# Performance work log

Measured on AMD Instinct MI355X. Metric: run time of the kernel, lower is better.

The kernel has to match this reference:

```python
import jax, jax.numpy as jnp
import numpy as np

N = 50000
E = 800000
IN_C = 128
OUT_C = 128
N_TYPES = 3
NEG_SLOPE = 0.2  # PyG GATConv default negative_slope


def setup_inputs() -> dict:
    key = jax.random.key(0)
    ks = jax.random.split(key, 10)
    x = jax.random.normal(ks[0], (N, IN_C), dtype=jnp.float32)
    edge_index = jax.random.randint(ks[1], (2, E), 0, N, dtype=jnp.int32)
    edge_type = jax.random.randint(ks[2], (E,), 0, N_TYPES, dtype=jnp.int32)
    node_type = jax.random.randint(ks[3], (N,), 0, 3, dtype=jnp.int32)
    s = 1.0 / np.sqrt(IN_C)
    emb_table = jax.random.normal(ks[4], (3, IN_C), dtype=jnp.float32)
    W = jax.random.normal(ks[5], (N_TYPES, IN_C, OUT_C), dtype=jnp.float32) * s
    att_src = jax.random.normal(ks[6], (N_TYPES, OUT_C), dtype=jnp.float32) * s
    att_dst = jax.random.normal(ks[7], (N_TYPES, OUT_C), dtype=jnp.float32) * s
    bias = jax.random.normal(ks[8], (N_TYPES, OUT_C), dtype=jnp.float32) * 0.01
    return {"x": x, "edge_index": edge_index, "edge_type": edge_type,
            "node_type": node_type, "emb_table": emb_table, "W": W,
            "att_src": att_src, "att_dst": att_dst, "bias": bias}


def reference(x, edge_index, edge_type, node_type, emb_table, W, att_src, att_dst, bias):
    # Eval mode: dropouts are identity. edge_index is non-empty -> GAT branch.
    n = x.shape[0]
    x = x + emb_table[node_type]  # node-type embedding add
    src, dst = edge_index[0], edge_index[1]
    out_sum = jnp.zeros((n, OUT_C), dtype=x.dtype)
    for t in range(N_TYPES):  # per-edge-type GATConv (heads=1, add_self_loops=True)
        xw = x @ W[t]                       # [N, out]
        a_s = xw @ att_src[t]               # [N] alpha_src per node
        a_d = xw @ att_dst[t]               # [N] alpha_dst per node
        mask = edge_type == t               # [E]
        e_raw = jax.nn.leaky_relu(a_s[src] + a_d[dst], NEG_SLOPE)  # [E]
        e_self = jax.nn.leaky_relu(a_s + a_d, NEG_SLOPE)           # [N] self-loop logit
        e_masked = jnp.where(mask, e_raw, -jnp.inf)
        m = jnp.maximum(jax.ops.segment_max(e_masked, dst, num_segments=n), e_self)
        m = jax.lax.stop_gradient(m)
        w_edge = jnp.where(mask, jnp.exp(e_raw - m[dst]), 0.0)     # [E]
        w_self = jnp.exp(e_self - m)                               # [N]
        denom = jax.ops.segment_sum(w_edge, dst, num_segments=n) + w_self
        num = jax.ops.segment_sum(w_edge[:, None] * xw[src], dst, num_segments=n) \
              + w_self[:, None] * xw
        out_sum = out_sum + num / denom[:, None] + bias[t]
        # (attention weights per type are w_edge/denom[dst]; only node output returned)
    return out_sum
```

## Files before the change

### kernel.cpp

```cpp
#include <hip/hip_runtime.h>
#include <math.h>

#define N_NODES 50000
#define N_EDGES 800000
#define C 128
#define NT 3
#define NEG 0.2f
#define CAP 64

typedef __attribute__((ext_vector_type(8))) short short8;
typedef __attribute__((ext_vector_type(4))) float f32x4;

__device__ __forceinline__ float leaky(float v) { return v > 0.f ? v : NEG * v; }

__device__ __forceinline__ unsigned short f2bf(float f) {
  unsigned int u = __float_as_uint(f);
  u = (u + 0x7FFFu + ((u >> 16) & 1u)) >> 16;
  return (unsigned short)u;
}
__device__ __forceinline__ float bf_lo(unsigned int w) { return __uint_as_float(w << 16); }
__device__ __forceinline__ float bf_hi(unsigned int w) { return __uint_as_float(w & 0xFFFF0000u); }

__global__ void k_x2(const float* __restrict__ x, const int* __restrict__ node_type,
                     const float* __restrict__ emb, unsigned short* __restrict__ x2b) {
  int i4 = blockIdx.x * 256 + threadIdx.x;
  if (i4 >= N_NODES * (C / 4)) return;
  int node = i4 >> 5;
  int q = i4 & 31;
  int nt = node_type[node];
  float4 xv = ((const float4*)x)[i4];
  float4 ev = ((const float4*)emb)[nt * 32 + q];
  ushort4 o;
  o.x = f2bf(xv.x + ev.x); o.y = f2bf(xv.y + ev.y);
  o.z = f2bf(xv.z + ev.z); o.w = f2bf(xv.w + ev.w);
  ((ushort4*)x2b)[i4] = o;
}

__global__ void k_wt(const float* __restrict__ W, unsigned short* __restrict__ Wt) {
  int n = blockIdx.x, t = blockIdx.y, k = threadIdx.x;
  Wt[((size_t)t * C + n) * C + k] = f2bf(W[((size_t)t * C + k) * C + n]);
}

__global__ void k_gemm(const unsigned short* __restrict__ x2b, const unsigned short* __restrict__ Wt,
                       unsigned short* __restrict__ xwb,
                       const float* __restrict__ att_src, const float* __restrict__ att_dst,
                       float* __restrict__ a_s, float2* __restrict__ ad_es) {
  __shared__ unsigned short As[64][136];
  __shared__ unsigned short Bs[128][136];
  const int tid = threadIdx.x;
  const int wid = tid >> 6, lane = tid & 63;
  const int m = lane & 15, quad = lane >> 4;
  const int row0 = blockIdx.x * 64;
  const int t = blockIdx.z;

#pragma unroll
  for (int it = 0; it < 4; ++it) {
    int c = tid + it * 256;
    int r = c >> 4, kc = c & 15;
    uint4 v = make_uint4(0, 0, 0, 0);
    if (row0 + r < N_NODES) v = *(const uint4*)(x2b + ((size_t)(row0 + r)) * C + kc * 8);
    *(uint4*)&As[r][kc * 8] = v;
  }
  const unsigned short* Wtt = Wt + (size_t)t * C * C;
#pragma unroll
  for (int it = 0; it < 8; ++it) {
    int c = tid + it * 256;
    int n = c >> 4, kc = c & 15;
    *(uint4*)&Bs[n][kc * 8] = *(const uint4*)(Wtt + (size_t)n * C + kc * 8);
  }
  __syncthreads();

  f32x4 acc[8] = {};
#pragma unroll
  for (int k0 = 0; k0 < 128; k0 += 32) {
    short8 a = *(const short8*)&As[wid * 16 + m][k0 + quad * 8];
#pragma unroll
    for (int j = 0; j < 8; ++j) {
      short8 b = *(const short8*)&Bs[j * 16 + m][k0 + quad * 8];
      acc[j] = __builtin_amdgcn_mfma_f32_16x16x32_bf16(a, b, acc[j], 0, 0, 0);
    }
  }

  float asv[8], adv[8];
#pragma unroll
  for (int j = 0; j < 8; ++j) {
    asv[j] = att_src[t * C + j * 16 + m];
    adv[j] = att_dst[t * C + j * 16 + m];
  }
  float ps[4] = {}, pd[4] = {};
#pragma unroll
  for (int j = 0; j < 8; ++j) {
#pragma unroll
    for (int reg = 0; reg < 4; ++reg) {
      int row = row0 + wid * 16 + quad * 4 + reg;
      float v = acc[j][reg];
      if (row < N_NODES) xwb[((size_t)t * N_NODES + row) * C + j * 16 + m] = f2bf(v);
      ps[reg] += v * asv[j];
      pd[reg] += v * adv[j];
    }
  }
#pragma unroll
  for (int off = 1; off < 16; off <<= 1) {
#pragma unroll
    for (int reg = 0; reg < 4; ++reg) {
      ps[reg] += __shfl_xor(ps[reg], off);
      pd[reg] += __shfl_xor(pd[reg], off);
    }
  }
  if (m == 0) {
#pragma unroll
    for (int reg = 0; reg < 4; ++reg) {
      int row = row0 + wid * 16 + quad * 4 + reg;
      if (row < N_NODES) {
        int idx = t * N_NODES + row;
        a_s[idx] = ps[reg];
        ad_es[idx] = make_float2(pd[reg], leaky(ps[reg] + pd[reg]));
      }
    }
  }
}

__global__ void k_edge(const int* __restrict__ ei, const int* __restrict__ etype,
                       const float* __restrict__ a_s, const float2* __restrict__ ad_es,
                       int* __restrict__ cnt, int2* __restrict__ buckets) {
  int e = blockIdx.x * 256 + threadIdx.x;
  if (e >= N_EDGES) return;
  int t = etype[e];
  int s = ei[e];
  int d = ei[N_EDGES + e];
  float as = a_s[t * N_NODES + s];
  float2 am = ad_es[t * N_NODES + d];
  float w = __expf(leaky(as + am.x) - am.y);
  int pos = atomicAdd(&cnt[d], 1);
  if (pos < CAP) buckets[(size_t)d * CAP + pos] = make_int2(t * N_NODES + s, __float_as_int(w));
}

__global__ void k_gather(const int* __restrict__ cnt, const int2* __restrict__ buckets,
                         const unsigned short* __restrict__ xwb,
                         const float* __restrict__ bias, float* __restrict__ out) {
  int wid = threadIdx.x >> 6;
  int lane = threadIdx.x & 63;
  int i = blockIdx.x * 4 + wid;
  if (i >= N_NODES) return;
  int n = cnt[i];
  if (n > CAP) n = CAP;

  int2 meta = make_int2(0, 0);
  if (lane < n) meta = buckets[(size_t)i * CAP + lane];

  int tl = meta.x >= 2 * N_NODES ? 2 : (meta.x >= N_NODES ? 1 : 0);
  float wl = __int_as_float(meta.y);
  float s0 = tl == 0 ? wl : 0.f;
  float s1 = tl == 1 ? wl : 0.f;
  float s2 = tl == 2 ? wl : 0.f;
#pragma unroll
  for (int off = 1; off < 64; off <<= 1) {
    s0 += __shfl_xor(s0, off);
    s1 += __shfl_xor(s1, off);
    s2 += __shfl_xor(s2, off);
  }
  float inv3[NT] = {1.f / (s0 + 1.f), 1.f / (s1 + 1.f), 1.f / (s2 + 1.f)};

  float acc0 = 0.f, acc1 = 0.f;
#pragma unroll
  for (int t = 0; t < NT; ++t) {
    int idx = t * N_NODES + i;
    float coef = inv3[t];
    unsigned int w = ((const unsigned int*)(xwb + (size_t)idx * C))[lane];
    float2 b2 = ((const float2*)(bias + t * C))[lane];
    acc0 += coef * bf_lo(w) + b2.x;
    acc1 += coef * bf_hi(w) + b2.y;
  }

  const unsigned int* xwu = (const unsigned int*)xwb;
  int j = 0;
  for (; j + 4 <= n; j += 4) {
    int i0 = __shfl(meta.x, j + 0), i1 = __shfl(meta.x, j + 1);
    int i2 = __shfl(meta.x, j + 2), i3 = __shfl(meta.x, j + 3);
    float w0 = __shfl(__int_as_float(meta.y), j + 0), w1 = __shfl(__int_as_float(meta.y), j + 1);
    float w2 = __shfl(__int_as_float(meta.y), j + 2), w3 = __shfl(__int_as_float(meta.y), j + 3);
    unsigned int v0 = xwu[(size_t)i0 * (C / 2) + lane];
    unsigned int v1 = xwu[(size_t)i1 * (C / 2) + lane];
    unsigned int v2 = xwu[(size_t)i2 * (C / 2) + lane];
    unsigned int v3 = xwu[(size_t)i3 * (C / 2) + lane];
    float c0 = w0 * inv3[i0 >= 2 * N_NODES ? 2 : (i0 >= N_NODES ? 1 : 0)];
    float c1 = w1 * inv3[i1 >= 2 * N_NODES ? 2 : (i1 >= N_NODES ? 1 : 0)];
    float c2 = w2 * inv3[i2 >= 2 * N_NODES ? 2 : (i2 >= N_NODES ? 1 : 0)];
    float c3 = w3 * inv3[i3 >= 2 * N_NODES ? 2 : (i3 >= N_NODES ? 1 : 0)];
    acc0 += c0 * bf_lo(v0) + c1 * bf_lo(v1) + c2 * bf_lo(v2) + c3 * bf_lo(v3);
    acc1 += c0 * bf_hi(v0) + c1 * bf_hi(v1) + c2 * bf_hi(v2) + c3 * bf_hi(v3);
  }
  for (; j < n; ++j) {
    int idx = __shfl(meta.x, j);
    float w = __shfl(__int_as_float(meta.y), j);
    float coef = w * inv3[idx >= 2 * N_NODES ? 2 : (idx >= N_NODES ? 1 : 0)];
    unsigned int v = xwu[(size_t)idx * (C / 2) + lane];
    acc0 += coef * bf_lo(v);
    acc1 += coef * bf_hi(v);
  }
  ((float2*)(out + (size_t)i * C))[lane] = make_float2(acc0, acc1);
}

extern "C" void kernel_launch(void* const* d_in, const int* in_sizes, int n_in,
                              void* d_out, int out_size, void* d_ws, size_t ws_size,
                              hipStream_t stream) {
  const float* x       = (const float*)d_in[0];
  const int* edge_idx  = (const int*)d_in[1];
  const int* edge_type = (const int*)d_in[2];
  const int* node_type = (const int*)d_in[3];
  const float* emb     = (const float*)d_in[4];
  const float* W       = (const float*)d_in[5];
  const float* att_src = (const float*)d_in[6];
  const float* att_dst = (const float*)d_in[7];
  const float* bias    = (const float*)d_in[8];
  float* out = (float*)d_out;

  unsigned short* xwb = (unsigned short*)d_ws;
  unsigned short* x2b = xwb + (size_t)NT * N_NODES * C;
  unsigned short* Wt  = x2b + (size_t)N_NODES * C;
  float*  a_s   = (float*)(Wt + (size_t)NT * C * C);
  float2* ad_es = (float2*)(a_s + (size_t)NT * N_NODES);
  int*    cnt   = (int*)(ad_es + (size_t)NT * N_NODES);
  int2*   buckets = (int2*)(cnt + N_NODES);

  hipMemsetAsync(cnt, 0, N_NODES * sizeof(int), stream);
  k_x2<<<(N_NODES * (C / 4) + 255) / 256, 256, 0, stream>>>(x, node_type, emb, x2b);
  k_wt<<<dim3(C, NT), C, 0, stream>>>(W, Wt);

  dim3 gg((N_NODES + 63) / 64, 1, NT);
  k_gemm<<<gg, 256, 0, stream>>>(x2b, Wt, xwb, att_src, att_dst, a_s, ad_es);

  k_edge<<<(N_EDGES + 255) / 256, 256, 0, stream>>>(edge_idx, edge_type, a_s, ad_es, cnt, buckets);

  k_gather<<<(N_NODES + 3) / 4, 256, 0, stream>>>(cnt, buckets, xwb, bias, out);
}
```

Measured before the change: 215.1 us.

## Move attention logit computation from edge kernel into gather kernel

The per-edge attention weight (exp of leaky logit minus self-loop term) is now computed in the gather kernel per lane, not in the edge-bucketing kernel. Buckets store only the source index instead of an int2 (index, weight), halving bucket traffic. The normalized coefficient is precomputed per lane and the inner gather loop is unrolled by 8 with partial accumulators. In exchange, the gather kernel does extra random reads of a_s and ad_es per node. The edge kernel also no longer waits on the GEMM outputs.

```diff
diff --git a/kernel.cpp b/kernel.cpp
--- a/kernel.cpp
+++ b/kernel.cpp
@@ -121,22 +121,19 @@
 }
 
 __global__ void k_edge(const int* __restrict__ ei, const int* __restrict__ etype,
-                       const float* __restrict__ a_s, const float2* __restrict__ ad_es,
-                       int* __restrict__ cnt, int2* __restrict__ buckets) {
+                       int* __restrict__ cnt, int* __restrict__ buckets) {
   int e = blockIdx.x * 256 + threadIdx.x;
   if (e >= N_EDGES) return;
   int t = etype[e];
   int s = ei[e];
   int d = ei[N_EDGES + e];
-  float as = a_s[t * N_NODES + s];
-  float2 am = ad_es[t * N_NODES + d];
-  float w = __expf(leaky(as + am.x) - am.y);
   int pos = atomicAdd(&cnt[d], 1);
-  if (pos < CAP) buckets[(size_t)d * CAP + pos] = make_int2(t * N_NODES + s, __float_as_int(w));
-}
-
-__global__ void k_gather(const int* __restrict__ cnt, const int2* __restrict__ buckets,
+  if (pos < CAP) buckets[(size_t)d * CAP + pos] = t * N_NODES + s;
+}
+
+__global__ void k_gather(const int* __restrict__ cnt, const int* __restrict__ buckets,
                          const unsigned short* __restrict__ xwb,
+                         const float* __restrict__ a_s, const float2* __restrict__ ad_es,
                          const float* __restrict__ bias, float* __restrict__ out) {
   int wid = threadIdx.x >> 6;
   int lane = threadIdx.x & 63;
@@ -145,11 +142,13 @@
   int n = cnt[i];
   if (n > CAP) n = CAP;
 
-  int2 meta = make_int2(0, 0);
-  if (lane < n) meta = buckets[(size_t)i * CAP + lane];
-
-  int tl = meta.x >= 2 * N_NODES ? 2 : (meta.x >= N_NODES ? 1 : 0);
-  float wl = __int_as_float(meta.y);
+  int idxl = 0;
+  if (lane < n) idxl = buckets[(size_t)i * CAP + lane];
+  int tl = idxl >= 2 * N_NODES ? 2 : (idxl >= N_NODES ? 1 : 0);
+  float as = a_s[idxl];
+  float2 am = ad_es[tl * N_NODES + i];
+  float wl = (lane < n) ? __expf(leaky(as + am.x) - am.y) : 0.f;
+
   float s0 = tl == 0 ? wl : 0.f;
   float s1 = tl == 1 ? wl : 0.f;
   float s2 = tl == 2 ? wl : 0.f;
@@ -160,6 +159,7 @@
     s2 += __shfl_xor(s2, off);
   }
   float inv3[NT] = {1.f / (s0 + 1.f), 1.f / (s1 + 1.f), 1.f / (s2 + 1.f)};
+  float wc = wl * inv3[tl];
 
   float acc0 = 0.f, acc1 = 0.f;
 #pragma unroll
@@ -174,29 +174,24 @@
 
   const unsigned int* xwu = (const unsigned int*)xwb;
   int j = 0;
-  for (; j + 4 <= n; j += 4) {
-    int i0 = __shfl(meta.x, j + 0), i1 = __shfl(meta.x, j + 1);
-    int i2 = __shfl(meta.x, j + 2), i3 = __shfl(meta.x, j + 3);
-    float w0 = __shfl(__int_as_float(meta.y), j + 0), w1 = __shfl(__int_as_float(meta.y), j + 1);
-    float w2 = __shfl(__int_as_float(meta.y), j + 2), w3 = __shfl(__int_as_float(meta.y), j + 3);
-    unsigned int v0 = xwu[(size_t)i0 * (C / 2) + lane];
-    unsigned int v1 = xwu[(size_t)i1 * (C / 2) + lane];
-    unsigned int v2 = xwu[(size_t)i2 * (C / 2) + lane];
-    unsigned int v3 = xwu[(size_t)i3 * (C / 2) + lane];
-    float c0 = w0 * inv3[i0 >= 2 * N_NODES ? 2 : (i0 >= N_NODES ? 1 : 0)];
-    float c1 = w1 * inv3[i1 >= 2 * N_NODES ? 2 : (i1 >= N_NODES ? 1 : 0)];
-    float c2 = w2 * inv3[i2 >= 2 * N_NODES ? 2 : (i2 >= N_NODES ? 1 : 0)];
-    float c3 = w3 * inv3[i3 >= 2 * N_NODES ? 2 : (i3 >= N_NODES ? 1 : 0)];
-    acc0 += c0 * bf_lo(v0) + c1 * bf_lo(v1) + c2 * bf_lo(v2) + c3 * bf_lo(v3);
-    acc1 += c0 * bf_hi(v0) + c1 * bf_hi(v1) + c2 * bf_hi(v2) + c3 * bf_hi(v3);
+  for (; j + 8 <= n; j += 8) {
+    float ac0 = 0.f, ac1 = 0.f;
+#pragma unroll
+    for (int k = 0; k < 8; ++k) {
+      int idx = __shfl(idxl, j + k);
+      float c = __shfl(wc, j + k);
+      unsigned int v = xwu[(size_t)idx * (C / 2) + lane];
+      ac0 += c * bf_lo(v);
+      ac1 += c * bf_hi(v);
+    }
+    acc0 += ac0; acc1 += ac1;
   }
   for (; j < n; ++j) {
-    int idx = __shfl(meta.x, j);
-    float w = __shfl(__int_as_float(meta.y), j);
-    float coef = w * inv3[idx >= 2 * N_NODES ? 2 : (idx >= N_NODES ? 1 : 0)];
+    int idx = __shfl(idxl, j);
+    float c = __shfl(wc, j);
     unsigned int v = xwu[(size_t)idx * (C / 2) + lane];
-    acc0 += coef * bf_lo(v);
-    acc1 += coef * bf_hi(v);
+    acc0 += c * bf_lo(v);
+    acc1 += c * bf_hi(v);
   }
   ((float2*)(out + (size_t)i * C))[lane] = make_float2(acc0, acc1);
 }
@@ -221,7 +216,7 @@
   float*  a_s   = (float*)(Wt + (size_t)NT * C * C);
   float2* ad_es = (float2*)(a_s + (size_t)NT * N_NODES);
   int*    cnt   = (int*)(ad_es + (size_t)NT * N_NODES);
-  int2*   buckets = (int2*)(cnt + N_NODES);
+  int*    buckets = (int*)(cnt + N_NODES);
 
   hipMemsetAsync(cnt, 0, N_NODES * sizeof(int), stream);
   k_x2<<<(N_NODES * (C / 4) + 255) / 256, 256, 0, stream>>>(x, node_type, emb, x2b);
@@ -230,7 +225,7 @@
   dim3 gg((N_NODES + 63) / 64, 1, NT);
   k_gemm<<<gg, 256, 0, stream>>>(x2b, Wt, xwb, att_src, att_dst, a_s, ad_es);
 
-  k_edge<<<(N_EDGES + 255) / 256, 256, 0, stream>>>(edge_idx, edge_type, a_s, ad_es, cnt, buckets);
-
-  k_gather<<<(N_NODES + 3) / 4, 256, 0, stream>>>(cnt, buckets, xwb, bias, out);
-}
+  k_edge<<<(N_EDGES + 255) / 256, 256, 0, stream>>>(edge_idx, edge_type, cnt, buckets);
+
+  k_gather<<<(N_NODES + 3) / 4, 256, 0, stream>>>(cnt, buckets, xwb, a_s, ad_es, bias, out);
+}
```

Result: slower. 221.1 us (+2.8%).
